# Optimization experiments

Measured on AMD Instinct MI355X. Metric: run time of the kernel, lower is better.

## Reference

```python
import jax, jax.numpy as jnp
import numpy as np

KSIZE = 7
SIGMA = 3.0
ALPHA = 0.1
POS_VAL_FOR_ALL_NEG = 5.0
NEG_VAL_FOR_ALL_POS = -5.0


def _gauss_kernel():
    x = jnp.arange(KSIZE, dtype=jnp.float32) - (KSIZE - 1) / 2.0
    pdf = jnp.exp(-0.5 * (x / SIGMA) ** 2)
    return pdf / pdf.sum()


def _gaussian_blur(img):
    # img: (B, C, H, W); separable 7x7 gaussian, reflect padding (torchvision behavior)
    B, C, H, W = img.shape
    k = _gauss_kernel()
    pad = KSIZE // 2
    x = jnp.pad(img, ((0, 0), (0, 0), (pad, pad), (pad, pad)), mode='reflect')
    x = x.reshape(B * C, 1, H + 2 * pad, W + 2 * pad)
    kh = k.reshape(1, 1, KSIZE, 1)
    kw = k.reshape(1, 1, 1, KSIZE)
    x = jax.lax.conv_general_dilated(x, kh, (1, 1), 'VALID')
    x = jax.lax.conv_general_dilated(x, kw, (1, 1), 'VALID')
    return x.reshape(B, C, H, W)


def _dup_map(x, mask, fallback):
    # x, mask: (L,). Gather x[mask] (original order) then tile to length L.
    # Stable argsort puts True(=selected) positions first in original order.
    L = x.shape[0]
    cnt = mask.sum()
    order = jnp.argsort(jnp.logical_not(mask))  # selected indices first, stable
    idx = order[jnp.arange(L) % jnp.maximum(cnt, 1)]
    return jnp.where(cnt == 0, jnp.float32(fallback), x[idx])


_dup_vmapped = jax.vmap(_dup_map, in_axes=(0, 0, None))


def _bce_with_logits(x, y):
    # mean( max(x,0) - x*y + log1p(exp(-|x|)) ) == mean( softplus(x) - x*y )
    return jnp.mean(jnp.logaddexp(0.0, x) - x * y)


def _forward(inp, tgt):
    B, C, H, W = inp.shape
    aug_sim_target = (_gaussian_blur(tgt * 255.0) > 0).astype(jnp.float32)

    L = H * W
    x = inp.reshape(B * C, L)
    t = tgt.reshape(B * C, L)
    a = aug_sim_target.reshape(B * C, L)

    # duplicated_pos: gather input at target>0, tile; fallback +5 if no positives
    pos_mask = t > 0
    dup_pos = _dup_vmapped(x, pos_mask, POS_VAL_FOR_ALL_NEG)

    # duplicated_false_pos: prefer (input>0 & ~aug_pos); else all negatives; else -5
    aug_pos = a > 0
    fp_mask = jnp.logical_and(x > 0, jnp.logical_not(aug_pos))
    neg_mask = jnp.logical_not(aug_pos)
    cnt_fp = fp_mask.sum(axis=1, keepdims=True)
    chosen_mask = jnp.where(cnt_fp > 0, fp_mask, neg_mask)
    dup_fp = _dup_vmapped(x, chosen_mask, NEG_VAL_FOR_ALL_POS)

    sim = dup_pos * x
    aug_sim = dup_pos * dup_fp

    sim_loss = _bce_with_logits(sim, t) + _bce_with_logits(dup_pos, jnp.ones_like(x))
    aug_sim_loss = _bce_with_logits(aug_sim, jnp.zeros_like(x))
    return sim_loss + ALPHA * aug_sim_loss


def setup_inputs() -> dict:
    key = jax.random.key(0)
    k1, k2 = jax.random.split(key)
    B, C, H, W = 16, 3, 512, 512
    inp = jax.random.normal(k1, (B, C, H, W), dtype=jnp.float32)
    tgt = jax.random.randint(k2, (B, C, H, W), 0, 2).astype(jnp.float32)
    return {"input": inp, "target": tgt}


def reference(input, target):
    return _forward(input, target)
```

## Files before the change

### kernel.cpp

```cpp
#include <hip/hip_runtime.h>
#include <math.h>

constexpr int W = 512;
constexpr int HIMG = 512;
constexpr int L = 1 << 18;
constexpr int LOG2L = 18;
constexpr int TPB = 256;
constexpr int TILE = 2048;
constexpr int TILES_PER_ROW = L / TILE;
constexpr int WORDS_PER_TILE = TILE / 64;
constexpr int SPB = 32;
constexpr int HALO = 3;
constexpr int HBUF = SPB + 2 * HALO;
constexpr int LBLK = 64;
constexpr int CHUNK = L / LBLK;
constexpr int G = CHUNK / (TPB * 4);
constexpr int JPB = 8 * TPB;

typedef unsigned long long ull;

__device__ __forceinline__ float softplus_f(float v) {
    return fmaxf(v, 0.0f) +
           0.6931471805599453f *
               __builtin_amdgcn_logf(1.0f + __builtin_amdgcn_exp2f(-fabsf(v) * 1.4426950408889634f));
}

__device__ __forceinline__ ull hdil7(ull prev, ull cur, ull next) {
    ull r = cur;
    r |= (cur >> 1) | (next << 63);
    r |= (cur >> 2) | (next << 62);
    r |= (cur >> 3) | (next << 61);
    r |= (cur << 1) | (prev >> 63);
    r |= (cur << 2) | (prev >> 62);
    r |= (cur << 3) | (prev >> 61);
    return r;
}

template <typename T>
__device__ __forceinline__ T sel8(const T* a, int k) {
    return k == 0 ? a[0] : k == 1 ? a[1] : k == 2 ? a[2] : k == 3 ? a[3]
         : k == 4 ? a[4] : k == 5 ? a[5] : k == 6 ? a[6] : a[7];
}

__global__ __launch_bounds__(TPB)
void fused_mask_kernel(const float* __restrict__ x, const float* __restrict__ t,
                       ull* __restrict__ mT, ull* __restrict__ mFp, ull* __restrict__ mNeg,
                       int* __restrict__ cPos, int* __restrict__ cFp, int* __restrict__ cNeg,
                       float* __restrict__ out) {
    if (blockIdx.x == 0 && threadIdx.x == 0) out[0] = 0.0f;
    int b = blockIdx.x;
    int img = b >> 4;
    int y0 = (b & 15) * SPB;
    int gs0 = img * HIMG + y0;

    __shared__ ull hbuf[HBUF][8];
    __shared__ ull tbuf[SPB][8];
    __shared__ ull xbuf[SPB][8];

    int lane = threadIdx.x & 63;
    int wv = threadIdx.x >> 6;
    int ylo = (y0 - HALO < 0) ? 0 : y0 - HALO;
    int yhi = (y0 + SPB - 1 + HALO > HIMG - 1) ? HIMG - 1 : y0 + SPB - 1 + HALO;

    for (int yl = ylo + wv; yl <= yhi; yl += 4) {
        int gbase = (img * HIMG + yl) * W;
        bool own = (yl >= y0) && (yl < y0 + SPB);
        ull wt[8], wx[8], h[8];
#pragma unroll
        for (int k = 0; k < 8; ++k) wt[k] = __ballot(t[gbase + k * 64 + lane] > 0.0f);
        if (own) {
#pragma unroll
            for (int k = 0; k < 8; ++k) wx[k] = __ballot(x[gbase + k * 64 + lane] > 0.0f);
        }
#pragma unroll
        for (int k = 0; k < 8; ++k) {
            ull cur = wt[k];
            ull prev = k ? wt[k - 1]
                         : ((((cur >> 1) & 1ull) << 63) | (((cur >> 2) & 1ull) << 62) |
                            (((cur >> 3) & 1ull) << 61));
            ull next = (k < 7) ? wt[k + 1]
                               : (((cur >> 62) & 1ull) | (((cur >> 61) & 1ull) << 1) |
                                  (((cur >> 60) & 1ull) << 2));
            h[k] = hdil7(prev, cur, next);
        }
        int hy = yl - (y0 - HALO);
        int k = lane & 7;
        if (lane < 8) {
            hbuf[hy][k] = sel8(h, k);
        } else if (own && lane < 16) {
            tbuf[yl - y0][k] = sel8(wt, k);
            mT[(img * HIMG + yl) * 8 + k] = sel8(wt, k);
        } else if (own && lane < 24) {
            xbuf[yl - y0][k] = sel8(wx, k);
        }
    }
    __syncthreads();

    int tid = threadIdx.x;
    int ys = tid >> 3;
    int c = tid & 7;
    int y = y0 + ys;
    ull wa = 0;
#pragma unroll
    for (int d = -3; d <= 3; ++d) {
        int yy = y + d;
        yy = yy < 0 ? -yy : (yy > HIMG - 1 ? 2 * (HIMG - 1) - yy : yy);
        wa |= hbuf[yy - (y0 - HALO)][c];
    }
    ull tw = tbuf[ys][c];
    ull fp = xbuf[ys][c] & ~wa;
    ull ng = ~wa;
    int gw = gs0 * 8 + tid;
    mFp[gw] = fp;
    mNeg[gw] = ng;
    int pT = __popcll(tw), pF = __popcll(fp), pN = __popcll(ng);
#pragma unroll
    for (int m = 1; m < 32; m <<= 1) {
        pT += __shfl_xor(pT, m, 64);
        pF += __shfl_xor(pF, m, 64);
        pN += __shfl_xor(pN, m, 64);
    }
    if ((lane & 31) == 0) {
        int tile = img * TILES_PER_ROW + (y0 >> 2) + (tid >> 5);
        cPos[tile] = pT; cFp[tile] = pF; cNeg[tile] = pN;
    }
}

__global__ void scan_kernel(const int* __restrict__ cPos, const int* __restrict__ cFp,
                            const int* __restrict__ cNeg,
                            int* __restrict__ oPos, int* __restrict__ oCh,
                            int* __restrict__ rCp, int* __restrict__ rCc,
                            ull* __restrict__ rMp, ull* __restrict__ rMc,
                            int* __restrict__ rUseFp) {
    int r = blockIdx.x;
    int tid = threadIdx.x;
    __shared__ int ssp[TILES_PER_ROW], ssf[TILES_PER_ROW], ssn[TILES_PER_ROW];
    int myp = cPos[r * TILES_PER_ROW + tid];
    int myf = cFp[r * TILES_PER_ROW + tid];
    int myn = cNeg[r * TILES_PER_ROW + tid];
    ssp[tid] = myp; ssf[tid] = myf; ssn[tid] = myn;
    __syncthreads();
    for (int off = 1; off < TILES_PER_ROW; off <<= 1) {
        int ap = 0, af = 0, an = 0;
        if (tid >= off) { ap = ssp[tid - off]; af = ssf[tid - off]; an = ssn[tid - off]; }
        __syncthreads();
        if (tid >= off) { ssp[tid] += ap; ssf[tid] += af; ssn[tid] += an; }
        __syncthreads();
    }
    int cp = ssp[TILES_PER_ROW - 1], cf = ssf[TILES_PER_ROW - 1], cn = ssn[TILES_PER_ROW - 1];
    bool useFp = cf > 0;
    int tile = r * TILES_PER_ROW + tid;
    oPos[tile] = ssp[tid] - myp;
    oCh[tile] = useFp ? (ssf[tid] - myf) : (ssn[tid] - myn);
    if (tid == 0) {
        int cc = useFp ? cf : cn;
        rCp[r] = cp; rCc[r] = cc; rUseFp[r] = useFp ? 1 : 0;
        ull dp_ = (ull)(cp > 0 ? cp : 1);
        ull dc_ = (ull)(cc > 0 ? cc : 1);
        rMp[r] = ((1ull << 40) + dp_ - 1) / dp_;
        rMc[r] = ((1ull << 40) + dc_ - 1) / dc_;
    }
}

__global__ __launch_bounds__(TPB)
void scatter_kernel(const float* __restrict__ x, const ull* __restrict__ mT,
                    const ull* __restrict__ mFp, const ull* __restrict__ mNeg,
                    const int* __restrict__ oPos, const int* __restrict__ oCh,
                    const int* __restrict__ rUseFp,
                    float* __restrict__ xp, float* __restrict__ xf) {
    int tile = blockIdx.x;
    int tid = threadIdx.x;
    int r = tile >> 7;
    bool useFp = rUseFp[r] != 0;
    int widx = tile * WORDS_PER_TILE + (tid >> 3);
    int shift = (tid & 7) * 8;
    unsigned bT = (unsigned)(mT[widx] >> shift) & 0xFF;
    ull chw = useFp ? mFp[widx] : mNeg[widx];
    unsigned bCh = (unsigned)(chw >> shift) & 0xFF;
    const float4* x4 = (const float4*)x;
    int b4 = tile * (TILE / 4) + tid * 2;
    float4 a = x4[b4], b = x4[b4 + 1];
    float xv[8] = {a.x, a.y, a.z, a.w, b.x, b.y, b.z, b.w};
    int p = __popc(bT), c = __popc(bCh);
    __shared__ int s[TPB];
    __shared__ float bufP[TILE], bufC[TILE];
    int v = p | (c << 16);
    s[tid] = v;
    __syncthreads();
    for (int off = 1; off < TPB; off <<= 1) {
        int add = tid >= off ? s[tid - off] : 0;
        __syncthreads();
        s[tid] += add;
        __syncthreads();
    }
    int excl = s[tid] - v;
    int ep = excl & 0xFFFF;
    int ec = excl >> 16;
#pragma unroll
    for (int e = 0; e < 8; ++e) {
        if ((bT >> e) & 1) bufP[ep++] = xv[e];
        if ((bCh >> e) & 1) bufC[ec++] = xv[e];
    }
    __syncthreads();
    int tot = s[TPB - 1];
    int P = tot & 0xFFFF, C = tot >> 16;
    int rL = r << LOG2L;
    int pbase = rL + oPos[tile];
    for (int i = tid; i < P; i += TPB) xp[pbase + i] = bufP[i];
    int cbase = rL + oCh[tile];
    for (int i = tid; i < C; i += TPB) xf[cbase + i] = bufC[i];
}

__global__ __launch_bounds__(TPB)
void loss_kernel(const float* __restrict__ x, const ull* __restrict__ mT,
                 const float* __restrict__ xp, const float* __restrict__ xf,
                 const int* __restrict__ rCp, const int* __restrict__ rCc,
                 const ull* __restrict__ rMp, const ull* __restrict__ rMc,
                 float* __restrict__ out, double inv_ntot) {
    int b = blockIdx.x;
    int r = b >> 6;
    int blk = b & 63;
    int rL = r << LOG2L;
    int cp = rCp[r], cc = rCc[r];
    const float* xr = x + rL;
    const float* xpr = xp + rL;
    const ull* mtr = mT + (rL >> 6);
    int tid = threadIdx.x;
    float local = 0.0f;

    if (cc == 0 && cp * 3 >= L) {
        for (int base = blk * JPB; base < cp; base += 64 * JPB) {
#pragma unroll
            for (int it = 0; it < 8; ++it) {
                int j = base + it * TPB + tid;
                if (j < cp) {
                    float dp = xpr[j];
                    int l2 = j + cp, l3 = l2 + cp;
                    bool b2 = l2 < L, b3 = l3 < L;
                    float x1 = xr[j];
                    float x2 = b2 ? xr[l2] : 0.0f;
                    float x3 = b3 ? xr[l3] : 0.0f;
                    unsigned t1 = (unsigned)(mtr[j >> 6] >> (j & 63)) & 1u;
                    unsigned t2 = b2 ? ((unsigned)(mtr[l2 >> 6] >> (l2 & 63)) & 1u) : 0u;
                    unsigned t3 = b3 ? ((unsigned)(mtr[l3 >> 6] >> (l3 & 63)) & 1u) : 0u;
                    float n = 1.0f + (b2 ? 1.0f : 0.0f) + (b3 ? 1.0f : 0.0f);
                    float sim1 = dp * x1, sim2 = dp * x2, sim3 = dp * x3;
                    float e = softplus_f(sim1) - (t1 ? sim1 : 0.0f);
                    e += b2 ? (softplus_f(sim2) - (t2 ? sim2 : 0.0f)) : 0.0f;
                    e += b3 ? (softplus_f(sim3) - (t3 ? sim3 : 0.0f)) : 0.0f;
                    e += n * (softplus_f(-dp) + 0.1f * softplus_f(-5.0f * dp));
                    local += e;
                }
            }
        }
    } else {
        int cb = blk * CHUNK;
        ull Mp = rMp[r], Mc = rMc[r];
        const float* xfr = xf + rL;
        const float4* x4 = (const float4*)(xr + cb);
#pragma unroll
        for (int g = 0; g < G; ++g) {
            int o4 = g * TPB + tid;
            unsigned l = (unsigned)(cb + (o4 << 2));
            float4 xv = x4[o4];
            unsigned tb = (unsigned)(mtr[l >> 6] >> (l & 63)) & 0xFu;
            float dps[4], dfs[4];
            if (cp > 0) {
                unsigned d = (unsigned)cp;
                unsigned q = (unsigned)(((ull)l * Mp) >> 40);
                unsigned m0 = l - q * d;
                unsigned m1 = m0 + 1; if (m1 == d) m1 = 0;
                unsigned m2 = m1 + 1; if (m2 == d) m2 = 0;
                unsigned m3 = m2 + 1; if (m3 == d) m3 = 0;
                dps[0] = xpr[m0]; dps[1] = xpr[m1]; dps[2] = xpr[m2]; dps[3] = xpr[m3];
            } else {
                dps[0] = dps[1] = dps[2] = dps[3] = 5.0f;
            }
            if (cc > 0) {
                unsigned d = (unsigned)cc;
                unsigned q = (unsigned)(((ull)l * Mc) >> 40);
                unsigned m0 = l - q * d;
                unsigned m1 = m0 + 1; if (m1 == d) m1 = 0;
                unsigned m2 = m1 + 1; if (m2 == d) m2 = 0;
                unsigned m3 = m2 + 1; if (m3 == d) m3 = 0;
                dfs[0] = xfr[m0]; dfs[1] = xfr[m1]; dfs[2] = xfr[m2]; dfs[3] = xfr[m3];
            } else {
                dfs[0] = dfs[1] = dfs[2] = dfs[3] = -5.0f;
            }
            float xs[4] = {xv.x, xv.y, xv.z, xv.w};
#pragma unroll
            for (int k = 0; k < 4; ++k) {
                float dp = dps[k];
                float sim = dp * xs[k];
                float e = softplus_f(sim) + softplus_f(-dp) + 0.1f * softplus_f(dp * dfs[k]);
                if ((tb >> k) & 1) e -= sim;
                local += e;
            }
        }
    }

#pragma unroll
    for (int m = 1; m < 64; m <<= 1) local += __shfl_xor(local, m, 64);
    __shared__ double sw[4];
    int lane = tid & 63, wv = tid >> 6;
    if (lane == 0) sw[wv] = (double)local;
    __syncthreads();
    if (tid == 0) {
        double s = sw[0] + sw[1] + sw[2] + sw[3];
        atomicAdd(out, (float)(s * inv_ntot));
    }
}

extern "C" void kernel_launch(void* const* d_in, const int* in_sizes, int n_in,
                              void* d_out, int out_size, void* d_ws, size_t ws_size,
                              hipStream_t stream) {
    const float* x = (const float*)d_in[0];
    const float* t = (const float*)d_in[1];
    float* out = (float*)d_out;

    int ntot = in_sizes[0];
    int R = ntot >> LOG2L;
    int numTiles = ntot / TILE;
    int nwords = ntot / 64;
    int nMaskBlk = ntot / (SPB * W);

    char* ws = (char*)d_ws;
    size_t off = 0;
    auto alloc = [&](size_t bytes) {
        size_t p = off;
        off = (off + bytes + 255) & ~(size_t)255;
        return (void*)(ws + p);
    };
    ull* mT   = (ull*)alloc((size_t)nwords * 8);
    ull* mFp  = (ull*)alloc((size_t)nwords * 8);
    ull* mNeg = (ull*)alloc((size_t)nwords * 8);
    int* cPos = (int*)alloc(numTiles * sizeof(int));
    int* cFp  = (int*)alloc(numTiles * sizeof(int));
    int* cNeg = (int*)alloc(numTiles * sizeof(int));
    int* oPos = (int*)alloc(numTiles * sizeof(int));
    int* oCh  = (int*)alloc(numTiles * sizeof(int));
    int* rCp = (int*)alloc(R * sizeof(int));
    int* rCc = (int*)alloc(R * sizeof(int));
    int* rUseFp = (int*)alloc(R * sizeof(int));
    ull* rMp = (ull*)alloc(R * sizeof(ull));
    ull* rMc = (ull*)alloc(R * sizeof(ull));
    float* xp = (float*)alloc((size_t)ntot * sizeof(float));
    float* xf = (float*)alloc((size_t)ntot * sizeof(float));

    fused_mask_kernel<<<nMaskBlk, TPB, 0, stream>>>(x, t, mT, mFp, mNeg, cPos, cFp, cNeg, out);
    scan_kernel<<<R, TILES_PER_ROW, 0, stream>>>(cPos, cFp, cNeg, oPos, oCh,
                                                 rCp, rCc, rMp, rMc, rUseFp);
    scatter_kernel<<<numTiles, TPB, 0, stream>>>(x, mT, mFp, mNeg, oPos, oCh, rUseFp, xp, xf);
    loss_kernel<<<R * LBLK, TPB, 0, stream>>>(x, mT, xp, xf, rCp, rCc, rMp, rMc, out,
                                              1.0 / (double)ntot);
}
```

Before: 190.7 us.

## Fuse fast-path loss into scatter kernel and accumulate per-row doubles

For rows where the chosen mask is empty and positives cover at least a third of the row, the loss is now computed directly in the scatter kernel from shared-memory compacted values. This avoids writing xp to global memory and reading it back in a separate loss kernel. The loss kernel becomes a fallback that exits early for such rows. Partial sums are accumulated per row in double via atomics, and a new single-thread finalize kernel adds the extra launch.

After: 179.2 us. 6.1% less time.

```diff
diff --git a/kernel.cpp b/kernel.cpp
--- a/kernel.cpp
+++ b/kernel.cpp
@@ -8,6 +8,7 @@
 constexpr int TPB = 256;
 constexpr int TILE = 2048;
 constexpr int TILES_PER_ROW = L / TILE;
+constexpr int WORDS_PER_ROW = L / 64;
 constexpr int WORDS_PER_TILE = TILE / 64;
 constexpr int SPB = 32;
 constexpr int HALO = 3;
@@ -15,7 +16,6 @@
 constexpr int LBLK = 64;
 constexpr int CHUNK = L / LBLK;
 constexpr int G = CHUNK / (TPB * 4);
-constexpr int JPB = 8 * TPB;
 
 typedef unsigned long long ull;
 
@@ -46,8 +46,8 @@
 void fused_mask_kernel(const float* __restrict__ x, const float* __restrict__ t,
                        ull* __restrict__ mT, ull* __restrict__ mFp, ull* __restrict__ mNeg,
                        int* __restrict__ cPos, int* __restrict__ cFp, int* __restrict__ cNeg,
-                       float* __restrict__ out) {
-    if (blockIdx.x == 0 && threadIdx.x == 0) out[0] = 0.0f;
+                       double* __restrict__ rowAcc) {
+    if (blockIdx.x == 0 && threadIdx.x < 48) rowAcc[threadIdx.x] = 0.0;
     int b = blockIdx.x;
     int img = b >> 4;
     int y0 = (b & 15) * SPB;
@@ -163,15 +163,18 @@
 }
 
 __global__ __launch_bounds__(TPB)
-void scatter_kernel(const float* __restrict__ x, const ull* __restrict__ mT,
-                    const ull* __restrict__ mFp, const ull* __restrict__ mNeg,
-                    const int* __restrict__ oPos, const int* __restrict__ oCh,
-                    const int* __restrict__ rUseFp,
-                    float* __restrict__ xp, float* __restrict__ xf) {
+void scatter_loss_kernel(const float* __restrict__ x, const ull* __restrict__ mT,
+                         const ull* __restrict__ mFp, const ull* __restrict__ mNeg,
+                         const int* __restrict__ oPos, const int* __restrict__ oCh,
+                         const int* __restrict__ rUseFp,
+                         const int* __restrict__ rCp, const int* __restrict__ rCc,
+                         float* __restrict__ xp, float* __restrict__ xf,
+                         double* __restrict__ rowAcc) {
     int tile = blockIdx.x;
     int tid = threadIdx.x;
     int r = tile >> 7;
     bool useFp = rUseFp[r] != 0;
+    int cp = rCp[r], cc = rCc[r];
     int widx = tile * WORDS_PER_TILE + (tid >> 3);
     int shift = (tid & 7) * 8;
     unsigned bT = (unsigned)(mT[widx] >> shift) & 0xFF;
@@ -205,109 +208,131 @@
     int tot = s[TPB - 1];
     int P = tot & 0xFFFF, C = tot >> 16;
     int rL = r << LOG2L;
-    int pbase = rL + oPos[tile];
-    for (int i = tid; i < P; i += TPB) xp[pbase + i] = bufP[i];
-    int cbase = rL + oCh[tile];
-    for (int i = tid; i < C; i += TPB) xf[cbase + i] = bufC[i];
+
+    bool fast = (cc == 0) && (cp * 3 >= L) && (cp > 0);
+    if (!fast) {
+        int pbase = rL + oPos[tile];
+        for (int i = tid; i < P; i += TPB) xp[pbase + i] = bufP[i];
+        int cbase = rL + oCh[tile];
+        for (int i = tid; i < C; i += TPB) xf[cbase + i] = bufC[i];
+        return;
+    }
+
+    const float* xr = x + rL;
+    const ull* mtr = mT + (rL >> 6);
+    int jb = oPos[tile];
+    float local = 0.0f;
+    for (int i = tid; i < P; i += TPB) {
+        int j = jb + i;
+        float dp = bufP[i];
+        float x1 = xr[j];
+        unsigned t1 = (unsigned)(mtr[j >> 6] >> (j & 63)) & 1u;
+        float sim1 = dp * x1;
+        float e = softplus_f(sim1) - (t1 ? sim1 : 0.0f);
+        float n = 1.0f;
+        int l2 = j + cp;
+        if (l2 < L) {
+            float x2 = xr[l2];
+            unsigned t2 = (unsigned)(mtr[l2 >> 6] >> (l2 & 63)) & 1u;
+            float sim2 = dp * x2;
+            e += softplus_f(sim2) - (t2 ? sim2 : 0.0f);
+            n += 1.0f;
+        }
+        int l3 = j + 2 * cp;
+        if (l3 < L) {
+            float x3 = xr[l3];
+            unsigned t3 = (unsigned)(mtr[l3 >> 6] >> (l3 & 63)) & 1u;
+            float sim3 = dp * x3;
+            e += softplus_f(sim3) - (t3 ? sim3 : 0.0f);
+            n += 1.0f;
+        }
+        e += n * (softplus_f(-dp) + 0.1f * softplus_f(-5.0f * dp));
+        local += e;
+    }
+#pragma unroll
+    for (int m = 1; m < 64; m <<= 1) local += __shfl_xor(local, m, 64);
+    __shared__ double sw[4];
+    int lane = tid & 63, wvi = tid >> 6;
+    if (lane == 0) sw[wvi] = (double)local;
+    __syncthreads();
+    if (tid == 0) atomicAdd(&rowAcc[r], sw[0] + sw[1] + sw[2] + sw[3]);
 }
 
 __global__ __launch_bounds__(TPB)
-void loss_kernel(const float* __restrict__ x, const ull* __restrict__ mT,
-                 const float* __restrict__ xp, const float* __restrict__ xf,
-                 const int* __restrict__ rCp, const int* __restrict__ rCc,
-                 const ull* __restrict__ rMp, const ull* __restrict__ rMc,
-                 float* __restrict__ out, double inv_ntot) {
+void loss_fallback_kernel(const float* __restrict__ x, const ull* __restrict__ mT,
+                          const float* __restrict__ xp, const float* __restrict__ xf,
+                          const int* __restrict__ rCp, const int* __restrict__ rCc,
+                          const ull* __restrict__ rMp, const ull* __restrict__ rMc,
+                          double* __restrict__ rowAcc) {
     int b = blockIdx.x;
     int r = b >> 6;
+    int cp = rCp[r], cc = rCc[r];
+    if (cc == 0 && cp * 3 >= L && cp > 0) return;
     int blk = b & 63;
     int rL = r << LOG2L;
-    int cp = rCp[r], cc = rCc[r];
     const float* xr = x + rL;
     const float* xpr = xp + rL;
+    const float* xfr = xf + rL;
     const ull* mtr = mT + (rL >> 6);
     int tid = threadIdx.x;
     float local = 0.0f;
-
-    if (cc == 0 && cp * 3 >= L) {
-        for (int base = blk * JPB; base < cp; base += 64 * JPB) {
-#pragma unroll
-            for (int it = 0; it < 8; ++it) {
-                int j = base + it * TPB + tid;
-                if (j < cp) {
-                    float dp = xpr[j];
-                    int l2 = j + cp, l3 = l2 + cp;
-                    bool b2 = l2 < L, b3 = l3 < L;
-                    float x1 = xr[j];
-                    float x2 = b2 ? xr[l2] : 0.0f;
-                    float x3 = b3 ? xr[l3] : 0.0f;
-                    unsigned t1 = (unsigned)(mtr[j >> 6] >> (j & 63)) & 1u;
-                    unsigned t2 = b2 ? ((unsigned)(mtr[l2 >> 6] >> (l2 & 63)) & 1u) : 0u;
-                    unsigned t3 = b3 ? ((unsigned)(mtr[l3 >> 6] >> (l3 & 63)) & 1u) : 0u;
-                    float n = 1.0f + (b2 ? 1.0f : 0.0f) + (b3 ? 1.0f : 0.0f);
-                    float sim1 = dp * x1, sim2 = dp * x2, sim3 = dp * x3;
-                    float e = softplus_f(sim1) - (t1 ? sim1 : 0.0f);
-                    e += b2 ? (softplus_f(sim2) - (t2 ? sim2 : 0.0f)) : 0.0f;
-                    e += b3 ? (softplus_f(sim3) - (t3 ? sim3 : 0.0f)) : 0.0f;
-                    e += n * (softplus_f(-dp) + 0.1f * softplus_f(-5.0f * dp));
-                    local += e;
-                }
-            }
-        }
-    } else {
-        int cb = blk * CHUNK;
-        ull Mp = rMp[r], Mc = rMc[r];
-        const float* xfr = xf + rL;
-        const float4* x4 = (const float4*)(xr + cb);
-#pragma unroll
-        for (int g = 0; g < G; ++g) {
-            int o4 = g * TPB + tid;
-            unsigned l = (unsigned)(cb + (o4 << 2));
-            float4 xv = x4[o4];
-            unsigned tb = (unsigned)(mtr[l >> 6] >> (l & 63)) & 0xFu;
-            float dps[4], dfs[4];
-            if (cp > 0) {
-                unsigned d = (unsigned)cp;
-                unsigned q = (unsigned)(((ull)l * Mp) >> 40);
-                unsigned m0 = l - q * d;
-                unsigned m1 = m0 + 1; if (m1 == d) m1 = 0;
-                unsigned m2 = m1 + 1; if (m2 == d) m2 = 0;
-                unsigned m3 = m2 + 1; if (m3 == d) m3 = 0;
-                dps[0] = xpr[m0]; dps[1] = xpr[m1]; dps[2] = xpr[m2]; dps[3] = xpr[m3];
-            } else {
-                dps[0] = dps[1] = dps[2] = dps[3] = 5.0f;
-            }
-            if (cc > 0) {
-                unsigned d = (unsigned)cc;
-                unsigned q = (unsigned)(((ull)l * Mc) >> 40);
-                unsigned m0 = l - q * d;
-                unsigned m1 = m0 + 1; if (m1 == d) m1 = 0;
-                unsigned m2 = m1 + 1; if (m2 == d) m2 = 0;
-                unsigned m3 = m2 + 1; if (m3 == d) m3 = 0;
-                dfs[0] = xfr[m0]; dfs[1] = xfr[m1]; dfs[2] = xfr[m2]; dfs[3] = xfr[m3];
-            } else {
-                dfs[0] = dfs[1] = dfs[2] = dfs[3] = -5.0f;
-            }
-            float xs[4] = {xv.x, xv.y, xv.z, xv.w};
-#pragma unroll
-            for (int k = 0; k < 4; ++k) {
-                float dp = dps[k];
-                float sim = dp * xs[k];
-                float e = softplus_f(sim) + softplus_f(-dp) + 0.1f * softplus_f(dp * dfs[k]);
-                if ((tb >> k) & 1) e -= sim;
-                local += e;
-            }
-        }
-    }
-
+    int cb = blk * CHUNK;
+    ull Mp = rMp[r], Mc = rMc[r];
+    const float4* x4 = (const float4*)(xr + cb);
+#pragma unroll
+    for (int g = 0; g < G; ++g) {
+        int o4 = g * TPB + tid;
+        unsigned l = (unsigned)(cb + (o4 << 2));
+        float4 xv = x4[o4];
+        unsigned tb = (unsigned)(mtr[l >> 6] >> (l & 63)) & 0xFu;
+        float dps[4], dfs[4];
+        if (cp > 0) {
+            unsigned d = (unsigned)cp;
+            unsigned q = (unsigned)(((ull)l * Mp) >> 40);
+            unsigned m0 = l - q * d;
+            unsigned m1 = m0 + 1; if (m1 == d) m1 = 0;
+            unsigned m2 = m1 + 1; if (m2 == d) m2 = 0;
+            unsigned m3 = m2 + 1; if (m3 == d) m3 = 0;
+            dps[0] = xpr[m0]; dps[1] = xpr[m1]; dps[2] = xpr[m2]; dps[3] = xpr[m3];
+        } else {
+            dps[0] = dps[1] = dps[2] = dps[3] = 5.0f;
+        }
+        if (cc > 0) {
+            unsigned d = (unsigned)cc;
+            unsigned q = (unsigned)(((ull)l * Mc) >> 40);
+            unsigned m0 = l - q * d;
+            unsigned m1 = m0 + 1; if (m1 == d) m1 = 0;
+            unsigned m2 = m1 + 1; if (m2 == d) m2 = 0;
+            unsigned m3 = m2 + 1; if (m3 == d) m3 = 0;
+            dfs[0] = xfr[m0]; dfs[1] = xfr[m1]; dfs[2] = xfr[m2]; dfs[3] = xfr[m3];
+        } else {
+            dfs[0] = dfs[1] = dfs[2] = dfs[3] = -5.0f;
+        }
+        float xs[4] = {xv.x, xv.y, xv.z, xv.w};
+#pragma unroll
+        for (int k = 0; k < 4; ++k) {
+            float dp = dps[k];
+            float sim = dp * xs[k];
+            float e = softplus_f(sim) + softplus_f(-dp) + 0.1f * softplus_f(dp * dfs[k]);
+            if ((tb >> k) & 1) e -= sim;
+            local += e;
+        }
+    }
 #pragma unroll
     for (int m = 1; m < 64; m <<= 1) local += __shfl_xor(local, m, 64);
     __shared__ double sw[4];
     int lane = tid & 63, wv = tid >> 6;
     if (lane == 0) sw[wv] = (double)local;
     __syncthreads();
-    if (tid == 0) {
-        double s = sw[0] + sw[1] + sw[2] + sw[3];
-        atomicAdd(out, (float)(s * inv_ntot));
+    if (tid == 0) atomicAdd(&rowAcc[r], sw[0] + sw[1] + sw[2] + sw[3]);
+}
+
+__global__ void finalize_kernel(const double* __restrict__ rowAcc, float* __restrict__ out,
+                                double inv_ntot, int R) {
+    if (threadIdx.x == 0) {
+        double s = 0.0;
+        for (int r = 0; r < R; ++r) s += rowAcc[r];
+        out[0] = (float)(s * inv_ntot);
     }
 }
 
@@ -331,6 +356,7 @@
         off = (off + bytes + 255) & ~(size_t)255;
         return (void*)(ws + p);
     };
+    double* rowAcc = (double*)alloc(R * sizeof(double));
     ull* mT   = (ull*)alloc((size_t)nwords * 8);
     ull* mFp  = (ull*)alloc((size_t)nwords * 8);
     ull* mNeg = (ull*)alloc((size_t)nwords * 8);
@@ -347,10 +373,13 @@
     float* xp = (float*)alloc((size_t)ntot * sizeof(float));
     float* xf = (float*)alloc((size_t)ntot * sizeof(float));
 
-    fused_mask_kernel<<<nMaskBlk, TPB, 0, stream>>>(x, t, mT, mFp, mNeg, cPos, cFp, cNeg, out);
+    fused_mask_kernel<<<nMaskBlk, TPB, 0, stream>>>(x, t, mT, mFp, mNeg, cPos, cFp, cNeg,
+                                                    rowAcc);
     scan_kernel<<<R, TILES_PER_ROW, 0, stream>>>(cPos, cFp, cNeg, oPos, oCh,
                                                  rCp, rCc, rMp, rMc, rUseFp);
-    scatter_kernel<<<numTiles, TPB, 0, stream>>>(x, mT, mFp, mNeg, oPos, oCh, rUseFp, xp, xf);
-    loss_kernel<<<R * LBLK, TPB, 0, stream>>>(x, mT, xp, xf, rCp, rCc, rMp, rMc, out,
-                                              1.0 / (double)ntot);
-}
+    scatter_loss_kernel<<<numTiles, TPB, 0, stream>>>(x, mT, mFp, mNeg, oPos, oCh, rUseFp,
+                                                      rCp, rCc, xp, xf, rowAcc);
+    loss_fallback_kernel<<<R * LBLK, TPB, 0, stream>>>(x, mT, xp, xf, rCp, rCc, rMp, rMc,
+                                                       rowAcc);
+    finalize_kernel<<<1, 64, 0, stream>>>(rowAcc, out, 1.0 / (double)ntot, R);
+}
```
